# Kernel tuning notes

Measured on AMD Instinct MI355X. Metric: run time of the kernel, lower is better.

Reference implementation:

```python
import jax, jax.numpy as jnp
import numpy as np

SAMPLE_RATE = 0.1
BINS = int(256 * SAMPLE_RATE)  # 25
KSIZE = 7
EPS = 1e-6


def _pascal_kernel_2d(ksize):
    # kornia get_pascal_kernel_2d(ksize, norm=True): outer product of binomial row, sum=1
    row = np.array([1.0, 6.0, 15.0, 20.0, 15.0, 6.0, 1.0], dtype=np.float32)
    row = row / row.sum()
    k2d = np.outer(row, row)
    return jnp.asarray(k2d, dtype=jnp.float32)


def _blur_pool2d(x, ksize=KSIZE):
    # kornia.filters.blur_pool2d: depthwise conv with pascal kernel, stride 2, zero pad ksize//2
    C = x.shape[1]
    k = jnp.broadcast_to(_pascal_kernel_2d(ksize).astype(x.dtype), (C, 1, ksize, ksize))
    pad = ksize // 2
    return jax.lax.conv_general_dilated(
        x, k, window_strides=(2, 2), padding=((pad, pad), (pad, pad)),
        feature_group_count=C, dimension_numbers=("NCHW", "OIHW", "NCHW"))


def _per_channel_hist(x, bins):
    # torch.histc(v, bins, 0, 1) per (b, c) plane: values outside [0,1] ignored,
    # value == 1 falls in last bin. Fused via one flat scatter-add.
    B, C, H, W = x.shape
    v = x.reshape(B * C, H * W)
    idx = jnp.clip(jnp.floor(v * bins).astype(jnp.int32), 0, bins - 1)
    valid = ((v >= 0.0) & (v <= 1.0)).astype(x.dtype)
    flat_idx = (jnp.arange(B * C, dtype=jnp.int32)[:, None] * bins + idx).reshape(-1)
    hist = jnp.zeros(B * C * bins, dtype=x.dtype).at[flat_idx].add(valid.reshape(-1))
    return hist.reshape(B, C, bins)


def setup_inputs() -> dict:
    key = jax.random.key(0)
    kx, ky = jax.random.split(key)
    B, C, H, W = 32, 3, 512, 512
    x = jax.random.uniform(kx, (B, C, H, W), dtype=jnp.float32)
    y = jax.random.uniform(ky, (B, C, H, W), dtype=jnp.float32)
    return {"x": x, "y": y}


def reference(x, y):
    hw = x.shape[-2] * x.shape[-1]  # original H*W (as in source)
    xb = _blur_pool2d(x)
    yb = _blur_pool2d(y)
    xh = _per_channel_hist(xb, BINS) / hw  # [B, C, BINS]
    yh = _per_channel_hist(yb, BINS) / hw
    # nn.CosineSimilarity(dim=0, eps=1e-6) applied per (b, c) vector pair
    dot = jnp.sum(xh * yh, axis=-1)
    nx = jnp.maximum(jnp.linalg.norm(xh, axis=-1), EPS)
    ny = jnp.maximum(jnp.linalg.norm(yh, axis=-1), EPS)
    cos = dot / (nx * ny)  # [B, C]
    return jnp.mean(cos)
```

## Files before the change

kernel.cpp:

```cpp
#include <hip/hip_runtime.h>

#define BINS 25
#define H 512
#define W 512
#define NPLANES 96
#define NSH 32
#define BPP 4
#define RING 6

typedef const __attribute__((address_space(1))) void* gvp;
typedef __attribute__((address_space(3))) void* lvp;

__global__ __launch_bounds__(256) void blur_hist(
        const float* __restrict__ x, const float* __restrict__ y,
        unsigned int* __restrict__ partial) {
    const int b = ((blockIdx.x & 7) * 96) + (blockIdx.x >> 3);
    const int z = b >> 2;
    const float* src = (z < NPLANES) ? x + (size_t)z * H * W
                                     : y + (size_t)(z - NPLANES) * H * W;

    __shared__ __align__(16) float ring[4][RING][512];
    __shared__ unsigned int sh[NSH * BINS];

    const int tid = threadIdx.x;
    if (tid < (NSH * BINS / 4))
        *(float4*)((float*)sh + 4 * tid) = make_float4(0.f, 0.f, 0.f, 0.f);
    __syncthreads();

    const int l  = tid & 63;
    const int wv = tid >> 6;
    const int S  = (b & 3) * 4 + wv;
    const int g0 = 32 * S - 3;

    float* const rbase = &ring[wv][0][0];

    auto STAGE = [&](int k, int sl) {
        int gy = g0 + k;
        gy = min(max(gy, 0), H - 1);
        const float* rp = src + (size_t)gy * W + 4 * l;
        float* lp = rbase + sl * 512;
        __builtin_amdgcn_global_load_lds((gvp)(rp),       (lvp)lp,         16, 0, 0);
        __builtin_amdgcn_global_load_lds((gvp)(rp + 256), (lvp)(lp + 256), 16, 0, 0);
    };

    const int p0 = max(2 * l - 1, 0);
    const int p1 = 2 * l;
    const int p2 = 2 * l + 1;
    const int p3 = min(2 * l + 2, 127);
    const float m0 = (l == 0)  ? 0.f : 1.f;
    const float m3 = (l == 63) ? 0.f : 1.f;

    const float w0 = 1.f/64.f, w1 = 6.f/64.f, w2 = 15.f/64.f, w3 = 20.f/64.f;

    auto HROW = [&](int k, int sl) -> float4 {
        const float* rp = rbase + sl * 512;
        const float4 qa = *(const float4*)(rp + 4 * p0);
        const float4 qb = *(const float4*)(rp + 4 * p1);
        const float4 qc = *(const float4*)(rp + 4 * p2);
        const float4 qd = *(const float4*)(rp + 4 * p3);
        const int gy = g0 + k;
        const float rm = ((unsigned)gy < (unsigned)H) ? 1.f : 0.f;
        float r1 = qa.y * m0, r2 = qa.z * m0, r3 = qa.w * m0;
        float r4 = qb.x, r5 = qb.y, r6 = qb.z, r7 = qb.w;
        float r8 = qc.x, r9 = qc.y, r10 = qc.z, r11 = qc.w;
        float r12 = qd.x * m3, r13 = qd.y * m3;
        float4 h;
        h.x = (w0*(r1 + r7)  + w1*(r2 + r6)  + w2*(r3 + r5)  + w3*r4)  * rm;
        h.y = (w0*(r3 + r9)  + w1*(r4 + r8)  + w2*(r5 + r7)  + w3*r6)  * rm;
        h.z = (w0*(r5 + r11) + w1*(r6 + r10) + w2*(r7 + r9)  + w3*r8)  * rm;
        h.w = (w0*(r7 + r13) + w1*(r8 + r12) + w2*(r9 + r11) + w3*r10) * rm;
        return h;
    };

    unsigned int* wh = sh + (tid & (NSH - 1)) * BINS;
    auto binit = [&](float v) {
        int bb = min((int)(v * 25.f), BINS - 1);
        atomicAdd(&wh[bb], 1u);
    };
    auto vout = [&](const float4& h0, const float4& h1, const float4& h2,
                    const float4& h3, const float4& h4, const float4& h5,
                    const float4& h6) {
        binit(w0*(h0.x+h6.x) + w1*(h1.x+h5.x) + w2*(h2.x+h4.x) + w3*h3.x);
        binit(w0*(h0.y+h6.y) + w1*(h1.y+h5.y) + w2*(h2.y+h4.y) + w3*h3.y);
        binit(w0*(h0.z+h6.z) + w1*(h1.z+h5.z) + w2*(h2.z+h4.z) + w3*h3.z);
        binit(w0*(h0.w+h6.w) + w1*(h1.w+h5.w) + w2*(h2.w+h4.w) + w3*h3.w);
    };

    STAGE(0, 0); STAGE(1, 1); STAGE(2, 2);
    STAGE(3, 3); STAGE(4, 4); STAGE(5, 5);
    asm volatile("s_waitcnt vmcnt(2)" ::: "memory");
    float4 h0 = HROW(0, 0), h1 = HROW(1, 1), h2 = HROW(2, 2),
           h3 = HROW(3, 3), h4 = HROW(4, 4);
    asm volatile("s_waitcnt lgkmcnt(0)" ::: "memory");
    STAGE(6, 0); STAGE(7, 1); STAGE(8, 2); STAGE(9, 3);

    float4 h5, h6;
    #pragma unroll
    for (int j = 0; j < 16; j++) {
        const int k5 = 2 * j + 5, k6 = 2 * j + 6;
        asm volatile("s_waitcnt vmcnt(6)" ::: "memory");
        h5 = HROW(k5, k5 % RING);
        h6 = HROW(k6, k6 % RING);
        asm volatile("s_waitcnt lgkmcnt(0)" ::: "memory");
        STAGE(2 * j + 10, (2 * j + 10) % RING);
        STAGE(2 * j + 11, (2 * j + 11) % RING);
        vout(h0, h1, h2, h3, h4, h5, h6);
        h0 = h2; h1 = h3; h2 = h4; h3 = h5; h4 = h6;
    }
    asm volatile("s_waitcnt vmcnt(0)" ::: "memory");
    __syncthreads();

    if (tid < BINS) {
        unsigned int acc = 0;
        #pragma unroll
        for (int g = 0; g < NSH; g++) acc += sh[g * BINS + tid];
        partial[b * BINS + tid] = acc;
    }
}

__global__ __launch_bounds__(64) void reduce_cos(
        const unsigned int* __restrict__ partial, float* __restrict__ out) {
    __shared__ float sa[BINS], sb[BINS];
    const int p = blockIdx.x;
    const int t = threadIdx.x;
    if (t < BINS) {
        unsigned int a = 0, bb = 0;
        #pragma unroll
        for (int j = 0; j < BPP; j++) {
            a  += partial[((size_t)p * BPP + j) * BINS + t];
            bb += partial[((size_t)(NPLANES + p) * BPP + j) * BINS + t];
        }
        sa[t] = (float)a;
        sb[t] = (float)bb;
    }
    __syncthreads();
    if (t == 0) {
        const float inv_hw = 1.0f / (float)(H * W);
        float dot = 0.f, nx = 0.f, ny = 0.f;
        for (int k = 0; k < BINS; k++) {
            float a = sa[k] * inv_hw;
            float c = sb[k] * inv_hw;
            dot += a * c;
            nx  += a * a;
            ny  += c * c;
        }
        nx = fmaxf(sqrtf(nx), 1e-6f);
        ny = fmaxf(sqrtf(ny), 1e-6f);
        atomicAdd(out, (dot / (nx * ny)) * (1.0f / (float)NPLANES));
    }
}

extern "C" void kernel_launch(void* const* d_in, const int* in_sizes, int n_in,
                              void* d_out, int out_size, void* d_ws, size_t ws_size,
                              hipStream_t stream) {
    const float* x = (const float*)d_in[0];
    const float* y = (const float*)d_in[1];
    float* out = (float*)d_out;

    unsigned int* partial = (unsigned int*)d_ws;

    hipMemsetAsync(out, 0, sizeof(float), stream);

    blur_hist<<<2 * NPLANES * BPP, 256, 0, stream>>>(x, y, partial);
    reduce_cos<<<NPLANES, 64, 0, stream>>>(partial, out);
}
```

Before: 222.1 us.

## Share row-staging across waves with a block-wide triple-buffered LDS ring

Rows are no longer staged per wave into private six-slot rings. Each wave now loads one half-row for all four waves' strips into a shared three-slot ring, and s_barrier calls keep the block in sync. The aim is to shrink LDS footprint per block (allowing more resident blocks) and spread global loads across waves. In exchange it adds block-wide barriers each iteration, coupling waves and possibly exposing load latency with shallower prefetch depth.

Result: no change. 221.1 us (-0.4%).

```diff
diff --git a/kernel.cpp b/kernel.cpp
--- a/kernel.cpp
+++ b/kernel.cpp
@@ -6,7 +6,6 @@
 #define NPLANES 96
 #define NSH 32
 #define BPP 4
-#define RING 6
 
 typedef const __attribute__((address_space(1))) void* gvp;
 typedef __attribute__((address_space(3))) void* lvp;
@@ -19,29 +18,30 @@
     const float* src = (z < NPLANES) ? x + (size_t)z * H * W
                                      : y + (size_t)(z - NPLANES) * H * W;
 
-    __shared__ __align__(16) float ring[4][RING][512];
+    __shared__ __align__(16) float ring[3][4][2][512];
     __shared__ unsigned int sh[NSH * BINS];
 
     const int tid = threadIdx.x;
+    const int l   = tid & 63;
+    const int wv  = tid >> 6;
+    const int sb  = (b & 3) * 4;
+    const int g0  = 32 * (sb + wv) - 3;
+    const int pr  = wv >> 1;
+    const int hf  = wv & 1;
+
+    auto STAGE = [&](int p, int slot) {
+        #pragma unroll
+        for (int k = 0; k < 4; ++k) {
+            int gy = 32 * (sb + k) - 3 + 2 * p + pr;
+            gy = min(max(gy, 0), H - 1);
+            const float* rp = src + (size_t)gy * W + hf * 256 + 4 * l;
+            __builtin_amdgcn_global_load_lds(
+                (gvp)rp, (lvp)&ring[slot][k][pr][hf * 256], 16, 0, 0);
+        }
+    };
+
     if (tid < (NSH * BINS / 4))
         *(float4*)((float*)sh + 4 * tid) = make_float4(0.f, 0.f, 0.f, 0.f);
-    __syncthreads();
-
-    const int l  = tid & 63;
-    const int wv = tid >> 6;
-    const int S  = (b & 3) * 4 + wv;
-    const int g0 = 32 * S - 3;
-
-    float* const rbase = &ring[wv][0][0];
-
-    auto STAGE = [&](int k, int sl) {
-        int gy = g0 + k;
-        gy = min(max(gy, 0), H - 1);
-        const float* rp = src + (size_t)gy * W + 4 * l;
-        float* lp = rbase + sl * 512;
-        __builtin_amdgcn_global_load_lds((gvp)(rp),       (lvp)lp,         16, 0, 0);
-        __builtin_amdgcn_global_load_lds((gvp)(rp + 256), (lvp)(lp + 256), 16, 0, 0);
-    };
 
     const int p0 = max(2 * l - 1, 0);
     const int p1 = 2 * l;
@@ -49,11 +49,10 @@
     const int p3 = min(2 * l + 2, 127);
     const float m0 = (l == 0)  ? 0.f : 1.f;
     const float m3 = (l == 63) ? 0.f : 1.f;
-
     const float w0 = 1.f/64.f, w1 = 6.f/64.f, w2 = 15.f/64.f, w3 = 20.f/64.f;
 
-    auto HROW = [&](int k, int sl) -> float4 {
-        const float* rp = rbase + sl * 512;
+    auto HROW = [&](int k) -> float4 {
+        const float* rp = &ring[(k >> 1) % 3][wv][k & 1][0];
         const float4 qa = *(const float4*)(rp + 4 * p0);
         const float4 qb = *(const float4*)(rp + 4 * p1);
         const float4 qc = *(const float4*)(rp + 4 * p2);
@@ -87,26 +86,32 @@
     };
 
     STAGE(0, 0); STAGE(1, 1); STAGE(2, 2);
-    STAGE(3, 3); STAGE(4, 4); STAGE(5, 5);
-    asm volatile("s_waitcnt vmcnt(2)" ::: "memory");
-    float4 h0 = HROW(0, 0), h1 = HROW(1, 1), h2 = HROW(2, 2),
-           h3 = HROW(3, 3), h4 = HROW(4, 4);
+    asm volatile("s_waitcnt vmcnt(0) lgkmcnt(0)" ::: "memory");
+    __builtin_amdgcn_s_barrier();
+    asm volatile("" ::: "memory");
+    float4 h0 = HROW(0), h1 = HROW(1), h2 = HROW(2),
+           h3 = HROW(3), h4 = HROW(4);
     asm volatile("s_waitcnt lgkmcnt(0)" ::: "memory");
-    STAGE(6, 0); STAGE(7, 1); STAGE(8, 2); STAGE(9, 3);
+    __builtin_amdgcn_s_barrier();
+    asm volatile("" ::: "memory");
+    STAGE(3, 0);
 
     float4 h5, h6;
     #pragma unroll
-    for (int j = 0; j < 16; j++) {
-        const int k5 = 2 * j + 5, k6 = 2 * j + 6;
-        asm volatile("s_waitcnt vmcnt(6)" ::: "memory");
-        h5 = HROW(k5, k5 % RING);
-        h6 = HROW(k6, k6 % RING);
+    for (int q = 0; q < 16; ++q) {
+        STAGE(q + 4, (q + 4) % 3);
+        asm volatile("s_waitcnt vmcnt(4)" ::: "memory");
+        __builtin_amdgcn_s_barrier();
+        asm volatile("" ::: "memory");
+        h5 = HROW(2 * q + 5);
+        h6 = HROW(2 * q + 6);
         asm volatile("s_waitcnt lgkmcnt(0)" ::: "memory");
-        STAGE(2 * j + 10, (2 * j + 10) % RING);
-        STAGE(2 * j + 11, (2 * j + 11) % RING);
         vout(h0, h1, h2, h3, h4, h5, h6);
         h0 = h2; h1 = h3; h2 = h4; h3 = h5; h4 = h6;
+        __builtin_amdgcn_s_barrier();
+        asm volatile("" ::: "memory");
     }
+
     asm volatile("s_waitcnt vmcnt(0)" ::: "memory");
     __syncthreads();
 
```

## Replace LDS ring staging with direct register loads and wave shuffles for halo

Applied to the files above, without the earlier changes.

Removes the global_load_lds ring buffer and instead has each lane load its 8 contiguous columns directly into registers in batches of 8 rows. Horizontal halo values now come from neighbouring lanes via __shfl_up/__shfl_down instead of overlapping LDS reads. This aims to eliminate LDS traffic and waitcnt-based ring synchronisation and to free LDS for occupancy. In exchange, latency hiding relies on batched register loads with higher register pressure, and the 32-byte per-lane loads may coalesce less well.

Result: no change. 219.9 us (-1.0%).

```diff
diff --git a/kernel.cpp b/kernel.cpp
--- a/kernel.cpp
+++ b/kernel.cpp
@@ -6,10 +6,6 @@
 #define NPLANES 96
 #define NSH 32
 #define BPP 4
-#define RING 6
-
-typedef const __attribute__((address_space(1))) void* gvp;
-typedef __attribute__((address_space(3))) void* lvp;
 
 __global__ __launch_bounds__(256) void blur_hist(
         const float* __restrict__ x, const float* __restrict__ y,
@@ -19,9 +15,7 @@
     const float* src = (z < NPLANES) ? x + (size_t)z * H * W
                                      : y + (size_t)(z - NPLANES) * H * W;
 
-    __shared__ __align__(16) float ring[4][RING][512];
     __shared__ unsigned int sh[NSH * BINS];
-
     const int tid = threadIdx.x;
     if (tid < (NSH * BINS / 4))
         *(float4*)((float*)sh + 4 * tid) = make_float4(0.f, 0.f, 0.f, 0.f);
@@ -32,38 +26,21 @@
     const int S  = (b & 3) * 4 + wv;
     const int g0 = 32 * S - 3;
 
-    float* const rbase = &ring[wv][0][0];
-
-    auto STAGE = [&](int k, int sl) {
-        int gy = g0 + k;
-        gy = min(max(gy, 0), H - 1);
-        const float* rp = src + (size_t)gy * W + 4 * l;
-        float* lp = rbase + sl * 512;
-        __builtin_amdgcn_global_load_lds((gvp)(rp),       (lvp)lp,         16, 0, 0);
-        __builtin_amdgcn_global_load_lds((gvp)(rp + 256), (lvp)(lp + 256), 16, 0, 0);
-    };
-
-    const int p0 = max(2 * l - 1, 0);
-    const int p1 = 2 * l;
-    const int p2 = 2 * l + 1;
-    const int p3 = min(2 * l + 2, 127);
     const float m0 = (l == 0)  ? 0.f : 1.f;
     const float m3 = (l == 63) ? 0.f : 1.f;
+    const float w0 = 1.f/64.f, w1 = 6.f/64.f, w2 = 15.f/64.f, w3 = 20.f/64.f;
+    const float* colp = src + 8 * l;
 
-    const float w0 = 1.f/64.f, w1 = 6.f/64.f, w2 = 15.f/64.f, w3 = 20.f/64.f;
-
-    auto HROW = [&](int k, int sl) -> float4 {
-        const float* rp = rbase + sl * 512;
-        const float4 qa = *(const float4*)(rp + 4 * p0);
-        const float4 qb = *(const float4*)(rp + 4 * p1);
-        const float4 qc = *(const float4*)(rp + 4 * p2);
-        const float4 qd = *(const float4*)(rp + 4 * p3);
+    auto HB = [&](const float4& q0, const float4& q1, int k) -> float4 {
+        const float r1  = __shfl_up(q1.y, 1) * m0;
+        const float r2  = __shfl_up(q1.z, 1) * m0;
+        const float r3  = __shfl_up(q1.w, 1) * m0;
+        const float r12 = __shfl_down(q0.x, 1) * m3;
+        const float r13 = __shfl_down(q0.y, 1) * m3;
+        const float r4 = q0.x, r5 = q0.y, r6 = q0.z, r7 = q0.w;
+        const float r8 = q1.x, r9 = q1.y, r10 = q1.z, r11 = q1.w;
         const int gy = g0 + k;
         const float rm = ((unsigned)gy < (unsigned)H) ? 1.f : 0.f;
-        float r1 = qa.y * m0, r2 = qa.z * m0, r3 = qa.w * m0;
-        float r4 = qb.x, r5 = qb.y, r6 = qb.z, r7 = qb.w;
-        float r8 = qc.x, r9 = qc.y, r10 = qc.z, r11 = qc.w;
-        float r12 = qd.x * m3, r13 = qd.y * m3;
         float4 h;
         h.x = (w0*(r1 + r7)  + w1*(r2 + r6)  + w2*(r3 + r5)  + w3*r4)  * rm;
         h.y = (w0*(r3 + r9)  + w1*(r4 + r8)  + w2*(r5 + r7)  + w3*r6)  * rm;
@@ -86,28 +63,35 @@
         binit(w0*(h0.w+h6.w) + w1*(h1.w+h5.w) + w2*(h2.w+h4.w) + w3*h3.w);
     };
 
-    STAGE(0, 0); STAGE(1, 1); STAGE(2, 2);
-    STAGE(3, 3); STAGE(4, 4); STAGE(5, 5);
-    asm volatile("s_waitcnt vmcnt(2)" ::: "memory");
-    float4 h0 = HROW(0, 0), h1 = HROW(1, 1), h2 = HROW(2, 2),
-           h3 = HROW(3, 3), h4 = HROW(4, 4);
-    asm volatile("s_waitcnt lgkmcnt(0)" ::: "memory");
-    STAGE(6, 0); STAGE(7, 1); STAGE(8, 2); STAGE(9, 3);
+    float4 Aq[8], Bq[8];
+    float4 hw[7];
 
-    float4 h5, h6;
-    #pragma unroll
-    for (int j = 0; j < 16; j++) {
-        const int k5 = 2 * j + 5, k6 = 2 * j + 6;
-        asm volatile("s_waitcnt vmcnt(6)" ::: "memory");
-        h5 = HROW(k5, k5 % RING);
-        h6 = HROW(k6, k6 % RING);
-        asm volatile("s_waitcnt lgkmcnt(0)" ::: "memory");
-        STAGE(2 * j + 10, (2 * j + 10) % RING);
-        STAGE(2 * j + 11, (2 * j + 11) % RING);
-        vout(h0, h1, h2, h3, h4, h5, h6);
-        h0 = h2; h1 = h3; h2 = h4; h3 = h5; h4 = h6;
+#define BATCH(RB, NB)                                                        \
+    _Pragma("unroll")                                                        \
+    for (int i2 = 0; i2 < (NB); ++i2) {                                      \
+        int gy = g0 + (RB) + i2;                                             \
+        gy = min(max(gy, 0), H - 1);                                         \
+        const float* rp = colp + (size_t)gy * W;                             \
+        Aq[i2] = *(const float4*)(rp);                                       \
+        Bq[i2] = *(const float4*)(rp + 4);                                   \
+    }                                                                        \
+    _Pragma("unroll")                                                        \
+    for (int i2 = 0; i2 < (NB); ++i2) {                                      \
+        const int k = (RB) + i2;                                             \
+        hw[k % 7] = HB(Aq[i2], Bq[i2], k);                                   \
+        if (k >= 6 && (k & 1) == 0)                                          \
+            vout(hw[(k - 6) % 7], hw[(k - 5) % 7], hw[(k - 4) % 7],          \
+                 hw[(k - 3) % 7], hw[(k - 2) % 7], hw[(k - 1) % 7],          \
+                 hw[k % 7]);                                                 \
     }
-    asm volatile("s_waitcnt vmcnt(0)" ::: "memory");
+
+    BATCH(0, 8)
+    BATCH(8, 8)
+    BATCH(16, 8)
+    BATCH(24, 8)
+    BATCH(32, 5)
+#undef BATCH
+
     __syncthreads();
 
     if (tid < BINS) {
```
